# Optimization experiments

Measured on AMD Instinct MI355X. Metric: run time of the kernel, lower is better.

## Reference

```python
import jax, jax.numpy as jnp
import numpy as np

C, W, H = 256, 64, 192
RECORD_LEN = np.array([5, 3, 4, 2, 5, 3, 4, 2], dtype=np.int64)  # sums to 28


def setup_inputs() -> dict:
    key = jax.random.key(0)
    total = int(RECORD_LEN.sum())
    x = jax.random.normal(key, (total, C, W, H), dtype=jnp.float32)
    record_len = jnp.asarray(RECORD_LEN)
    return {"x": x, "record_len": record_len}


def _group_attention(xx):
    # xx: [L, C, W, H] -> per-pixel self-attention over the L agents, d_model = C
    L = xx.shape[0]
    q = xx.reshape(L, C, W * H).transpose(2, 0, 1)          # [N=W*H, L, C]
    score = jnp.einsum('nlc,nmc->nlm', q, q) / jnp.sqrt(jnp.float32(C))
    attn = jax.nn.softmax(score, axis=-1)                    # [N, L, L]
    # original keeps only ego agent (row 0) of the context
    ctx0 = jnp.einsum('nm,nmc->nc', attn[:, 0, :], q)        # [N, C]
    out = ctx0.T.reshape(1, C, W, H)
    attn_maps = attn.transpose(1, 2, 0).reshape(L, L, W, H)
    return out, attn_maps


def reference(x, record_len):
    rl = np.asarray(record_len)  # static ragged lengths
    offsets = np.concatenate([[0], np.cumsum(rl)])
    outs = []
    attn_last = None
    for i in range(len(rl)):  # small fixed number of ragged groups
        xx = x[int(offsets[i]):int(offsets[i + 1])]
        out_i, attn_last = _group_attention(xx)
        outs.append(out_i)
    # matches torch: returns fused ego features per scene + attn of LAST group
    return jnp.concatenate(outs, axis=0), attn_last
```

## Files before the change

kernel.cpp:

```cpp
#include <hip/hip_runtime.h>
#include <hip/hip_bf16.h>
#include <math.h>

#define C_DIM 256
#define W_DIM 64
#define H_DIM 192
#define WH (W_DIM * H_DIM)
#define NGROUPS 8
#define BLOCKS_PER_GROUP (WH / 256)

template <int L, bool WRITE_ATTN>
__device__ __forceinline__ void att_group_body(
    const float* __restrict__ xg,
    float* __restrict__ out,
    float* __restrict__ attn_out,
    int n)
{
    constexpr int NTRI = L * (L + 1) / 2;
    float s[NTRI];
#pragma unroll
    for (int i = 0; i < NTRI; ++i) s[i] = 0.0f;

#pragma unroll 4
    for (int c = 0; c < C_DIM; ++c) {
        float v[L];
#pragma unroll
        for (int l = 0; l < L; ++l)
            v[l] = xg[(l * C_DIM + c) * WH + n];
        int idx = 0;
#pragma unroll
        for (int l = 0; l < L; ++l)
#pragma unroll
            for (int m = l; m < L; ++m)
                s[idx++] += v[l] * v[m];
    }

    const float scale = 0.0625f;

    float p0[L];
    float mx = -INFINITY;
#pragma unroll
    for (int m = 0; m < L; ++m) {
        p0[m] = s[m] * scale;
        mx = fmaxf(mx, p0[m]);
    }
    float sum = 0.0f;
#pragma unroll
    for (int m = 0; m < L; ++m) {
        p0[m] = __expf(p0[m] - mx);
        sum += p0[m];
    }
    const float inv = 1.0f / sum;
#pragma unroll
    for (int m = 0; m < L; ++m) p0[m] *= inv;

    if constexpr (WRITE_ATTN) {
        float g[L][L];
        int idx = 0;
#pragma unroll
        for (int l = 0; l < L; ++l)
#pragma unroll
            for (int m = l; m < L; ++m) {
                const float v = s[idx++] * scale;
                g[l][m] = v;
                g[m][l] = v;
            }
#pragma unroll
        for (int l = 0; l < L; ++l) {
            float mx2 = -INFINITY;
#pragma unroll
            for (int m = 0; m < L; ++m) mx2 = fmaxf(mx2, g[l][m]);
            float e[L];
            float sm = 0.0f;
#pragma unroll
            for (int m = 0; m < L; ++m) {
                e[m] = __expf(g[l][m] - mx2);
                sm += e[m];
            }
            const float iv = 1.0f / sm;
#pragma unroll
            for (int m = 0; m < L; ++m)
                attn_out[(l * L + m) * WH + n] = e[m] * iv;
        }
    }

#pragma unroll 4
    for (int c = 0; c < C_DIM; ++c) {
        float acc = 0.0f;
#pragma unroll
        for (int m = 0; m < L; ++m)
            acc += p0[m] * xg[(m * C_DIM + c) * WH + n];
        out[c * WH + n] = acc;
    }
}

__global__ __launch_bounds__(256) void att_fused_kernel(
    const float* __restrict__ x,
    float* __restrict__ out0,
    float* __restrict__ attn)
{
    const int b = blockIdx.x;
    const int g = b / BLOCKS_PER_GROUP;
    const int bn = b - g * BLOCKS_PER_GROUP;
    const int n = bn * 256 + threadIdx.x;

    const int offs[NGROUPS] = {0, 5, 8, 12, 14, 19, 22, 26};
    const int lens[NGROUPS] = {5, 3, 4, 2, 5, 3, 4, 2};

    const float* xg = x + (size_t)offs[g] * C_DIM * WH;
    float* og = out0 + (size_t)g * C_DIM * WH;

    switch (lens[g]) {
        case 5: att_group_body<5, false>(xg, og, nullptr, n); break;
        case 4: att_group_body<4, false>(xg, og, nullptr, n); break;
        case 3: att_group_body<3, false>(xg, og, nullptr, n); break;
        case 2:
            if (g == NGROUPS - 1)
                att_group_body<2, true>(xg, og, attn, n);
            else
                att_group_body<2, false>(xg, og, nullptr, n);
            break;
    }
}

extern "C" void kernel_launch(void* const* d_in, const int* in_sizes, int n_in,
                              void* d_out, int out_size, void* d_ws, size_t ws_size,
                              hipStream_t stream) {
    const float* x = (const float*)d_in[0];
    float* out0 = (float*)d_out;
    float* attn = out0 + (size_t)NGROUPS * C_DIM * WH;

    const dim3 grid(NGROUPS * BLOCKS_PER_GROUP);
    const dim3 block(256);
    att_fused_kernel<<<grid, block, 0, stream>>>(x, out0, attn);
}
```

Measured before the change: 563.2 us.

## Split channel reduction across warps per pixel tile with LDS reduction

Each block now handles 64 pixels, with its four wavefronts each summing a quarter of the channels. Partial Gram sums are combined through LDS, one wavefront computes the softmax, and every wavefront then writes its channel slice of the output. This gives four times as many blocks and shorter serial loops per thread, which should improve latency hiding for this bandwidth-bound kernel. The cost is two block barriers, LDS traffic, and reduction work done by only one wavefront. Launch bounds also request occupancy of six blocks.

```diff
diff --git a/kernel.cpp b/kernel.cpp
--- a/kernel.cpp
+++ b/kernel.cpp
@@ -7,26 +7,42 @@
 #define H_DIM 192
 #define WH (W_DIM * H_DIM)
 #define NGROUPS 8
-#define BLOCKS_PER_GROUP (WH / 256)
+
+#define NL 64
+#define NCHUNK 4
+#define CCHUNK (C_DIM / NCHUNK)
+#define BLOCKS_PER_GROUP (WH / NL)
+#define MAX_NTRI 15
+#define MAX_L 5
+
+#define LDS_P0_OFF (NCHUNK * MAX_NTRI * NL)
+#define LDS_FLOATS (LDS_P0_OFF + MAX_L * NL)
 
 template <int L, bool WRITE_ATTN>
 __device__ __forceinline__ void att_group_body(
     const float* __restrict__ xg,
     float* __restrict__ out,
     float* __restrict__ attn_out,
-    int n)
+    float* lds, int n0)
 {
     constexpr int NTRI = L * (L + 1) / 2;
+    const int tid = threadIdx.x;
+    const int n_local = tid & (NL - 1);
+    const int chunk = tid >> 6;
+    const int n = n0 + n_local;
+    const int c0 = chunk * CCHUNK;
+
     float s[NTRI];
 #pragma unroll
     for (int i = 0; i < NTRI; ++i) s[i] = 0.0f;
 
-#pragma unroll 4
-    for (int c = 0; c < C_DIM; ++c) {
+#pragma unroll 2
+    for (int cc = 0; cc < CCHUNK; ++cc) {
+        const int c = c0 + cc;
         float v[L];
 #pragma unroll
         for (int l = 0; l < L; ++l)
-            v[l] = xg[(l * C_DIM + c) * WH + n];
+            v[l] = xg[((size_t)(l * C_DIM + c)) * WH + n];
         int idx = 0;
 #pragma unroll
         for (int l = 0; l < L; ++l)
@@ -35,74 +51,98 @@
                 s[idx++] += v[l] * v[m];
     }
 
+#pragma unroll
+    for (int t = 0; t < NTRI; ++t)
+        lds[(chunk * NTRI + t) * NL + n_local] = s[t];
+    __syncthreads();
+
     const float scale = 0.0625f;
 
-    float p0[L];
-    float mx = -INFINITY;
+    if (tid < NL) {
+        float tot[NTRI];
 #pragma unroll
-    for (int m = 0; m < L; ++m) {
-        p0[m] = s[m] * scale;
-        mx = fmaxf(mx, p0[m]);
-    }
-    float sum = 0.0f;
+        for (int t = 0; t < NTRI; ++t) {
+            float a = 0.0f;
 #pragma unroll
-    for (int m = 0; m < L; ++m) {
-        p0[m] = __expf(p0[m] - mx);
-        sum += p0[m];
-    }
-    const float inv = 1.0f / sum;
+            for (int k = 0; k < NCHUNK; ++k)
+                a += lds[(k * NTRI + t) * NL + tid];
+            tot[t] = a * scale;
+        }
+
+        float p0[L];
+        float mx = -INFINITY;
 #pragma unroll
-    for (int m = 0; m < L; ++m) p0[m] *= inv;
+        for (int m = 0; m < L; ++m) mx = fmaxf(mx, tot[m]);
+        float sum = 0.0f;
+#pragma unroll
+        for (int m = 0; m < L; ++m) {
+            p0[m] = __expf(tot[m] - mx);
+            sum += p0[m];
+        }
+        const float inv = 1.0f / sum;
+#pragma unroll
+        for (int m = 0; m < L; ++m)
+            lds[LDS_P0_OFF + m * NL + tid] = p0[m] * inv;
 
-    if constexpr (WRITE_ATTN) {
-        float g[L][L];
-        int idx = 0;
+        if constexpr (WRITE_ATTN) {
+            float g[L][L];
+            int idx = 0;
 #pragma unroll
-        for (int l = 0; l < L; ++l)
+            for (int l = 0; l < L; ++l)
 #pragma unroll
-            for (int m = l; m < L; ++m) {
-                const float v = s[idx++] * scale;
-                g[l][m] = v;
-                g[m][l] = v;
+                for (int m = l; m < L; ++m) {
+                    g[l][m] = tot[idx];
+                    g[m][l] = tot[idx];
+                    ++idx;
+                }
+#pragma unroll
+            for (int l = 0; l < L; ++l) {
+                float mx2 = -INFINITY;
+#pragma unroll
+                for (int m = 0; m < L; ++m) mx2 = fmaxf(mx2, g[l][m]);
+                float e[L];
+                float sm = 0.0f;
+#pragma unroll
+                for (int m = 0; m < L; ++m) {
+                    e[m] = __expf(g[l][m] - mx2);
+                    sm += e[m];
+                }
+                const float iv = 1.0f / sm;
+#pragma unroll
+                for (int m = 0; m < L; ++m)
+                    attn_out[((size_t)(l * L + m)) * WH + n0 + tid] = e[m] * iv;
             }
-#pragma unroll
-        for (int l = 0; l < L; ++l) {
-            float mx2 = -INFINITY;
-#pragma unroll
-            for (int m = 0; m < L; ++m) mx2 = fmaxf(mx2, g[l][m]);
-            float e[L];
-            float sm = 0.0f;
-#pragma unroll
-            for (int m = 0; m < L; ++m) {
-                e[m] = __expf(g[l][m] - mx2);
-                sm += e[m];
-            }
-            const float iv = 1.0f / sm;
-#pragma unroll
-            for (int m = 0; m < L; ++m)
-                attn_out[(l * L + m) * WH + n] = e[m] * iv;
         }
     }
+    __syncthreads();
+
+    float p[L];
+#pragma unroll
+    for (int m = 0; m < L; ++m)
+        p[m] = lds[LDS_P0_OFF + m * NL + n_local];
 
 #pragma unroll 4
-    for (int c = 0; c < C_DIM; ++c) {
+    for (int cc = 0; cc < CCHUNK; ++cc) {
+        const int c = c0 + cc;
         float acc = 0.0f;
 #pragma unroll
         for (int m = 0; m < L; ++m)
-            acc += p0[m] * xg[(m * C_DIM + c) * WH + n];
-        out[c * WH + n] = acc;
+            acc += p[m] * xg[((size_t)(m * C_DIM + c)) * WH + n];
+        out[(size_t)c * WH + n] = acc;
     }
 }
 
-__global__ __launch_bounds__(256) void att_fused_kernel(
+__global__ __launch_bounds__(256, 6) void att_fused_kernel(
     const float* __restrict__ x,
     float* __restrict__ out0,
     float* __restrict__ attn)
 {
+    __shared__ float lds[LDS_FLOATS];
+
     const int b = blockIdx.x;
     const int g = b / BLOCKS_PER_GROUP;
     const int bn = b - g * BLOCKS_PER_GROUP;
-    const int n = bn * 256 + threadIdx.x;
+    const int n0 = bn * NL;
 
     const int offs[NGROUPS] = {0, 5, 8, 12, 14, 19, 22, 26};
     const int lens[NGROUPS] = {5, 3, 4, 2, 5, 3, 4, 2};
@@ -111,14 +151,14 @@
     float* og = out0 + (size_t)g * C_DIM * WH;
 
     switch (lens[g]) {
-        case 5: att_group_body<5, false>(xg, og, nullptr, n); break;
-        case 4: att_group_body<4, false>(xg, og, nullptr, n); break;
-        case 3: att_group_body<3, false>(xg, og, nullptr, n); break;
+        case 5: att_group_body<5, false>(xg, og, nullptr, lds, n0); break;
+        case 4: att_group_body<4, false>(xg, og, nullptr, lds, n0); break;
+        case 3: att_group_body<3, false>(xg, og, nullptr, lds, n0); break;
         case 2:
             if (g == NGROUPS - 1)
-                att_group_body<2, true>(xg, og, attn, n);
+                att_group_body<2, true>(xg, og, attn, lds, n0);
             else
-                att_group_body<2, false>(xg, og, nullptr, n);
+                att_group_body<2, false>(xg, og, nullptr, lds, n0);
             break;
     }
 }
```

Result: slower. 574.7 us (+2.0%).
